# Kernel optimization log

Measured on AMD Instinct MI355X. Metric: run time of the kernel, lower is better.

The kernel has to match this reference:

```python
import jax, jax.numpy as jnp
import numpy as np

IN_F, OUT_F, TASK_D, RANK, HID = 1024, 1024, 256, 8, 64
ALPHA = 8.0
SCALING = ALPHA / RANK  # 1.0


def setup_inputs() -> dict:
    key = jax.random.key(0)
    ks = jax.random.split(key, 12)
    s = 0.02
    return {
        "x": jax.random.normal(ks[0], (4, 2048, IN_F), dtype=jnp.float32),
        "base_out": jax.random.normal(ks[1], (4, 2048, OUT_F), dtype=jnp.float32),
        "task_emb": jax.random.normal(ks[2], (4, TASK_D), dtype=jnp.float32),
        # gen_a MLP: Linear(task_dim->hid) + GELU + Linear(hid->out*r)
        "Wa1": jax.random.normal(ks[3], (HID, TASK_D), dtype=jnp.float32) * s,
        "ba1": jnp.zeros((HID,), dtype=jnp.float32),
        "Wa2": jax.random.normal(ks[4], (OUT_F * RANK, HID), dtype=jnp.float32) * s,
        "ba2": jnp.zeros((OUT_F * RANK,), dtype=jnp.float32),
        # gen_b MLP: Linear(task_dim->hid) + GELU + Linear(hid->r*in)
        "Wb1": jax.random.normal(ks[5], (HID, TASK_D), dtype=jnp.float32) * s,
        "bb1": jnp.zeros((HID,), dtype=jnp.float32),
        "Wb2": jax.random.normal(ks[6], (RANK * IN_F, HID), dtype=jnp.float32) * s,
        "bb2": jnp.zeros((RANK * IN_F,), dtype=jnp.float32),
    }


def reference(x, base_out, task_emb, Wa1, ba1, Wa2, ba2, Wb1, bb1, Wb2, bb2):
    lead = x.shape[:-1]
    x2d = x.reshape(-1, IN_F)                      # (b_eff, in)
    b_eff = x2d.shape[0]
    # broadcast task_emb to b_eff rows (repeat + trim, as in torch)
    B = task_emb.shape[0]
    reps = (b_eff + B - 1) // B
    task_eff = jnp.tile(task_emb, (reps, 1))[:b_eff]  # (b_eff, task_dim)

    gelu = lambda t: jax.nn.gelu(t, approximate=False)
    h_a = gelu(task_eff @ Wa1.T + ba1)
    vec_a = h_a @ Wa2.T + ba2                      # (b_eff, out*r)
    h_b = gelu(task_eff @ Wb1.T + bb1)
    vec_b = h_b @ Wb2.T + bb2                      # (b_eff, r*in)

    a = vec_a.reshape(b_eff, OUT_F, RANK)
    b = vec_b.reshape(b_eff, RANK, IN_F)

    # dropout p=0 (eval): x passes through
    tmp = jnp.einsum('bi,bri->br', x2d, b)         # (b_eff, r)
    y_delta = jnp.einsum('br,bor->bo', tmp, a)     # (b_eff, out)
    y = base_out.reshape(-1, OUT_F) + SCALING * y_delta
    return y.reshape(*lead, OUT_F)
```

## Files before the change

### kernel.cpp

```cpp
#include <hip/hip_runtime.h>
#include <math.h>

#define IN_F   1024
#define OUT_F  1024
#define TASK_D 256
#define RANK   8
#define HID    64

__device__ __forceinline__ float gelu_exact(float v) {
    return 0.5f * v * (1.0f + erff(v * 0.70710678118654752f));
}

__global__ __launch_bounds__(256) void gen_kernel(
    const float* __restrict__ task_emb,
    const float* __restrict__ Wa1, const float* __restrict__ ba1,
    const float* __restrict__ Wa2, const float* __restrict__ ba2,
    const float* __restrict__ Wb1, const float* __restrict__ bb1,
    const float* __restrict__ Wb2, const float* __restrict__ bb2,
    float* __restrict__ vec_a_t, float* __restrict__ vec_b)
{
    const int gen = blockIdx.x >> 8;
    const int blk = blockIdx.x & 255;
    const float* __restrict__ W1 = gen ? Wb1 : Wa1;
    const float* __restrict__ b1 = gen ? bb1 : ba1;
    const float* __restrict__ W2 = gen ? Wb2 : Wa2;
    const float* __restrict__ b2 = gen ? bb2 : ba2;

    __shared__ float hs[4][HID];
    {
        const int j = threadIdx.x >> 2;
        const int t = threadIdx.x & 3;
        const float4* te = (const float4*)(task_emb + t * TASK_D);
        const float4* w  = (const float4*)(W1 + j * TASK_D);
        float acc = 0.f;
        #pragma unroll
        for (int d = 0; d < TASK_D / 4; ++d) {
            float4 a = te[d], b = w[d];
            acc += a.x * b.x + a.y * b.y + a.z * b.z + a.w * b.w;
        }
        hs[t][j] = gelu_exact(acc + b1[j]);
    }
    __syncthreads();

    const int lrow = threadIdx.x >> 3;
    const int q    = threadIdx.x & 7;
    const int o    = blk * 32 + lrow;

    const float4* w2 = (const float4*)(W2 + (size_t)o * HID + q * 8);
    float acc0 = 0.f, acc1 = 0.f, acc2 = 0.f, acc3 = 0.f;
    #pragma unroll
    for (int k = 0; k < 2; ++k) {
        float4 w = w2[k];
        const int kb = q * 8 + k * 4;
        acc0 += hs[0][kb] * w.x + hs[0][kb+1] * w.y + hs[0][kb+2] * w.z + hs[0][kb+3] * w.w;
        acc1 += hs[1][kb] * w.x + hs[1][kb+1] * w.y + hs[1][kb+2] * w.z + hs[1][kb+3] * w.w;
        acc2 += hs[2][kb] * w.x + hs[2][kb+1] * w.y + hs[2][kb+2] * w.z + hs[2][kb+3] * w.w;
        acc3 += hs[3][kb] * w.x + hs[3][kb+1] * w.y + hs[3][kb+2] * w.z + hs[3][kb+3] * w.w;
    }
    #pragma unroll
    for (int off = 1; off <= 4; off <<= 1) {
        acc0 += __shfl_xor(acc0, off, 64);
        acc1 += __shfl_xor(acc1, off, 64);
        acc2 += __shfl_xor(acc2, off, 64);
        acc3 += __shfl_xor(acc3, off, 64);
    }
    if (q == 0) {
        const float bb = b2[o];
        float v[4] = { acc0 + bb, acc1 + bb, acc2 + bb, acc3 + bb };
        if (gen == 0) {
            const int oo = o >> 3, r = o & 7;
            #pragma unroll
            for (int t = 0; t < 4; ++t)
                vec_a_t[t * (RANK * OUT_F) + r * OUT_F + oo] = v[t];
        } else {
            #pragma unroll
            for (int t = 0; t < 4; ++t)
                vec_b[t * (RANK * IN_F) + o] = v[t];
        }
    }
}

__global__ __launch_bounds__(256, 6) void apply_kernel(
    const float* __restrict__ x, const float* __restrict__ base_out,
    const float* __restrict__ vec_a_t, const float* __restrict__ vec_b,
    float* __restrict__ out, int blocks_per_task)
{
    const int t    = blockIdx.x / blocks_per_task;
    const int g    = blockIdx.x % blocks_per_task;
    const int wave = threadIdx.x >> 6;
    const int ln   = threadIdx.x & 63;

    __shared__ float tmps[4][RANK];

    {
        const int row = t + 4 * (g * 4 + wave);
        const float* __restrict__ xr = x + (size_t)row * IN_F;
        const float* __restrict__ bt = vec_b + (size_t)t * (RANK * IN_F);

        float4 xv[4];
        #pragma unroll
        for (int c = 0; c < 4; ++c)
            xv[c] = *(const float4*)(xr + c * 256 + ln * 4);

        float acc[RANK];
        #pragma unroll
        for (int r = 0; r < RANK; ++r) acc[r] = 0.f;

        #pragma unroll
        for (int c = 0; c < 4; ++c) {
            const int k = c * 256 + ln * 4;
            #pragma unroll
            for (int r = 0; r < RANK; ++r) {
                const float4 bv = *(const float4*)(bt + r * IN_F + k);
                acc[r] += xv[c].x * bv.x + xv[c].y * bv.y
                        + xv[c].z * bv.z + xv[c].w * bv.w;
            }
        }

        #pragma unroll
        for (int off = 1; off <= 32; off <<= 1) {
            #pragma unroll
            for (int r = 0; r < RANK; ++r)
                acc[r] += __shfl_xor(acc[r], off, 64);
        }

        if (ln == 0) {
            #pragma unroll
            for (int r = 0; r < RANK; ++r)
                tmps[wave][r] = acc[r];
        }
    }
    __syncthreads();

    const int o = threadIdx.x * 4;
    const float* __restrict__ at = vec_a_t + (size_t)t * (RANK * OUT_F);

    float4 af[RANK];
    #pragma unroll
    for (int r = 0; r < RANK; ++r)
        af[r] = *(const float4*)(at + r * OUT_F + o);

    float4 bo[4];
    #pragma unroll
    for (int i = 0; i < 4; ++i) {
        const int row = t + 4 * (g * 4 + i);
        bo[i] = *(const float4*)(base_out + (size_t)row * OUT_F + o);
    }

    #pragma unroll
    for (int i = 0; i < 4; ++i) {
        const int row = t + 4 * (g * 4 + i);
        float4 rv = bo[i];
        #pragma unroll
        for (int r = 0; r < RANK; ++r) {
            const float s = tmps[i][r];
            rv.x += s * af[r].x;
            rv.y += s * af[r].y;
            rv.z += s * af[r].z;
            rv.w += s * af[r].w;
        }
        *(float4*)(out + (size_t)row * OUT_F + o) = rv;
    }
}

extern "C" void kernel_launch(void* const* d_in, const int* in_sizes, int n_in,
                              void* d_out, int out_size, void* d_ws, size_t ws_size,
                              hipStream_t stream) {
    const float* x        = (const float*)d_in[0];
    const float* base_out = (const float*)d_in[1];
    const float* task_emb = (const float*)d_in[2];
    const float* Wa1      = (const float*)d_in[3];
    const float* ba1      = (const float*)d_in[4];
    const float* Wa2      = (const float*)d_in[5];
    const float* ba2      = (const float*)d_in[6];
    const float* Wb1      = (const float*)d_in[7];
    const float* bb1      = (const float*)d_in[8];
    const float* Wb2      = (const float*)d_in[9];
    const float* bb2      = (const float*)d_in[10];
    float* out = (float*)d_out;

    float* vec_a_t = (float*)d_ws;
    float* vec_b   = vec_a_t + 4 * RANK * OUT_F;

    const int b_eff = in_sizes[0] / IN_F;

    gen_kernel<<<512, 256, 0, stream>>>(task_emb, Wa1, ba1, Wa2, ba2,
                                        Wb1, bb1, Wb2, bb2, vec_a_t, vec_b);

    const int nblk = b_eff / 4;
    apply_kernel<<<nblk, 256, 0, stream>>>(x, base_out, vec_a_t, vec_b, out,
                                           nblk / 4);
}
```

Measured before the change: 151.3 us.

## Stage vec_b in LDS and process eight rows per block in apply kernel

Each block now copies the per-task 32 KB vec_b slice into shared memory once, and every wave reuses it for two rows, instead of each wave streaming vec_b from global/L2. Blocks cover eight rows instead of four, halving the grid and doubling reuse of the vec_a fragments. The cost is 32 KB of LDS per block and lower launch-bounds occupancy, plus an extra barrier after the staging copy.

```diff
diff --git a/kernel.cpp b/kernel.cpp
--- a/kernel.cpp
+++ b/kernel.cpp
@@ -80,7 +80,7 @@
     }
 }
 
-__global__ __launch_bounds__(256, 6) void apply_kernel(
+__global__ __launch_bounds__(256, 4) void apply_kernel(
     const float* __restrict__ x, const float* __restrict__ base_out,
     const float* __restrict__ vec_a_t, const float* __restrict__ vec_b,
     float* __restrict__ out, int blocks_per_task)
@@ -90,76 +90,94 @@
     const int wave = threadIdx.x >> 6;
     const int ln   = threadIdx.x & 63;
 
-    __shared__ float tmps[4][RANK];
+    __shared__ float bs[RANK * IN_F];
+    __shared__ float tmps[8][RANK];
 
     {
-        const int row = t + 4 * (g * 4 + wave);
-        const float* __restrict__ xr = x + (size_t)row * IN_F;
-        const float* __restrict__ bt = vec_b + (size_t)t * (RANK * IN_F);
-
-        float4 xv[4];
-        #pragma unroll
-        for (int c = 0; c < 4; ++c)
-            xv[c] = *(const float4*)(xr + c * 256 + ln * 4);
-
-        float acc[RANK];
-        #pragma unroll
-        for (int r = 0; r < RANK; ++r) acc[r] = 0.f;
-
-        #pragma unroll
-        for (int c = 0; c < 4; ++c) {
-            const int k = c * 256 + ln * 4;
-            #pragma unroll
-            for (int r = 0; r < RANK; ++r) {
-                const float4 bv = *(const float4*)(bt + r * IN_F + k);
-                acc[r] += xv[c].x * bv.x + xv[c].y * bv.y
-                        + xv[c].z * bv.z + xv[c].w * bv.w;
-            }
-        }
-
-        #pragma unroll
-        for (int off = 1; off <= 32; off <<= 1) {
-            #pragma unroll
-            for (int r = 0; r < RANK; ++r)
-                acc[r] += __shfl_xor(acc[r], off, 64);
-        }
-
-        if (ln == 0) {
-            #pragma unroll
-            for (int r = 0; r < RANK; ++r)
-                tmps[wave][r] = acc[r];
-        }
-    }
-    __syncthreads();
+        const float4* __restrict__ src =
+            (const float4*)(vec_b + (size_t)t * (RANK * IN_F));
+        float4* dst = (float4*)bs;
+        #pragma unroll
+        for (int i = 0; i < 8; ++i)
+            dst[threadIdx.x + 256 * i] = src[threadIdx.x + 256 * i];
+    }
 
     const int o = threadIdx.x * 4;
     const float* __restrict__ at = vec_a_t + (size_t)t * (RANK * OUT_F);
-
     float4 af[RANK];
     #pragma unroll
     for (int r = 0; r < RANK; ++r)
         af[r] = *(const float4*)(at + r * OUT_F + o);
 
-    float4 bo[4];
-    #pragma unroll
-    for (int i = 0; i < 4; ++i) {
-        const int row = t + 4 * (g * 4 + i);
-        bo[i] = *(const float4*)(base_out + (size_t)row * OUT_F + o);
-    }
-
-    #pragma unroll
-    for (int i = 0; i < 4; ++i) {
-        const int row = t + 4 * (g * 4 + i);
-        float4 rv = bo[i];
-        #pragma unroll
-        for (int r = 0; r < RANK; ++r) {
-            const float s = tmps[i][r];
-            rv.x += s * af[r].x;
-            rv.y += s * af[r].y;
-            rv.z += s * af[r].z;
-            rv.w += s * af[r].w;
-        }
-        *(float4*)(out + (size_t)row * OUT_F + o) = rv;
+    __syncthreads();
+
+    {
+        const int j0 = g * 8 + wave * 2;
+        float4 xv[2][4];
+        #pragma unroll
+        for (int i = 0; i < 2; ++i) {
+            const int row = t + 4 * (j0 + i);
+            const float* __restrict__ xr = x + (size_t)row * IN_F;
+            #pragma unroll
+            for (int c = 0; c < 4; ++c)
+                xv[i][c] = *(const float4*)(xr + c * 256 + ln * 4);
+        }
+        #pragma unroll
+        for (int i = 0; i < 2; ++i) {
+            float acc[RANK];
+            #pragma unroll
+            for (int r = 0; r < RANK; ++r) acc[r] = 0.f;
+            #pragma unroll
+            for (int c = 0; c < 4; ++c) {
+                const int k = c * 256 + ln * 4;
+                #pragma unroll
+                for (int r = 0; r < RANK; ++r) {
+                    const float4 bv = *(const float4*)(bs + r * IN_F + k);
+                    acc[r] += xv[i][c].x * bv.x + xv[i][c].y * bv.y
+                            + xv[i][c].z * bv.z + xv[i][c].w * bv.w;
+                }
+            }
+            #pragma unroll
+            for (int off = 1; off <= 32; off <<= 1) {
+                #pragma unroll
+                for (int r = 0; r < RANK; ++r)
+                    acc[r] += __shfl_xor(acc[r], off, 64);
+            }
+            if (ln == 0) {
+                #pragma unroll
+                for (int r = 0; r < RANK; ++r)
+                    tmps[wave * 2 + i][r] = acc[r];
+            }
+        }
+    }
+    __syncthreads();
+
+    #pragma unroll
+    for (int ii = 0; ii < 2; ++ii) {
+        float4 bo[4];
+        #pragma unroll
+        for (int i = 0; i < 4; ++i) {
+            const int row = t + 4 * (g * 8 + ii * 4 + i);
+            bo[i] = *(const float4*)(base_out + (size_t)row * OUT_F + o);
+        }
+        #pragma unroll
+        for (int i = 0; i < 4; ++i) {
+            const int lrow = ii * 4 + i;
+            const int row  = t + 4 * (g * 8 + lrow);
+            const float4 t0 = *(const float4*)&tmps[lrow][0];
+            const float4 t1 = *(const float4*)&tmps[lrow][4];
+            const float s[RANK] = { t0.x, t0.y, t0.z, t0.w,
+                                    t1.x, t1.y, t1.z, t1.w };
+            float4 rv = bo[i];
+            #pragma unroll
+            for (int r = 0; r < RANK; ++r) {
+                rv.x += s[r] * af[r].x;
+                rv.y += s[r] * af[r].y;
+                rv.z += s[r] * af[r].z;
+                rv.w += s[r] * af[r].w;
+            }
+            *(float4*)(out + (size_t)row * OUT_F + o) = rv;
+        }
     }
 }
 
@@ -187,7 +205,7 @@
     gen_kernel<<<512, 256, 0, stream>>>(task_emb, Wa1, ba1, Wa2, ba2,
                                         Wb1, bb1, Wb2, bb2, vec_a_t, vec_b);
 
-    const int nblk = b_eff / 4;
+    const int nblk = b_eff / 8;
     apply_kernel<<<nblk, 256, 0, stream>>>(x, base_out, vec_a_t, vec_b, out,
                                            nblk / 4);
 }
```

Measured after the change: 152.2 us. Within noise of the previous version (+0.5%).
